# Kernel tuning notes

Hardware: AMD Instinct MI355X
Metric: run time of the kernel (lower is better)

Reference implementation:

```python
import jax, jax.numpy as jnp
import numpy as np

T, B, V, D, H, C = 2048, 32, 50257, 512, 768, 10


def setup_inputs() -> dict:
    key = jax.random.key(0)
    ks = jax.random.split(key, 11)
    s = 0.02
    return {
        "x": jax.random.randint(ks[0], (T, B), 0, V),
        "embed_table": jax.random.normal(ks[1], (V, D), jnp.float32) * s,
        "W_x": jax.random.normal(ks[2], (H, D), jnp.float32) * s,
        "W_f": jax.random.normal(ks[3], (H, D), jnp.float32) * s,
        "b_f": jax.random.normal(ks[4], (H,), jnp.float32) * s,
        "W_r": jax.random.normal(ks[5], (H, D), jnp.float32) * s,
        "b_r": jax.random.normal(ks[6], (H,), jnp.float32) * s,
        "W_cx": jax.random.normal(ks[7], (H, D), jnp.float32) * s,
        "b_cx": jax.random.normal(ks[8], (H,), jnp.float32) * s,
        "W_out": jax.random.normal(ks[9], (C, H), jnp.float32) * s,
        "b_out": jax.random.normal(ks[10], (C,), jnp.float32) * s,
    }


def reference(x, embed_table, W_x, W_f, b_f, W_r, b_r, W_cx, b_cx, W_out, b_out):
    # Embedding lookup: [T, B, D]
    e = embed_table[x]
    # Precompute all gate projections for every timestep (batched GEMMs).
    xp = jnp.einsum("tbd,hd->tbh", e, W_x)                 # x_t projection
    f = jax.nn.sigmoid(jnp.einsum("tbd,hd->tbh", e, W_f) + b_f)   # forget gate
    r = jax.nn.sigmoid(jnp.einsum("tbd,hd->tbh", e, W_r) + b_r)   # reset gate
    cx = jnp.einsum("tbd,hd->tbh", e, W_cx) + b_cx                # highway path

    c0 = jnp.zeros((B, H), e.dtype)  # init_hidden: zeros

    def step(c, inp):
        f_t, xp_t, r_t, cx_t = inp
        c = f_t * c + (1.0 - f_t) * xp_t
        h = r_t * jnp.tanh(c) + (1.0 - r_t) * cx_t
        return c, h

    _, ht = jax.lax.scan(step, c0, (f, xp, r, cx))  # ht: [T, B, H]

    # tanh -> max-pool over time -> tanh -> classifier
    pooled = jnp.max(jnp.tanh(ht), axis=0)          # [B, H]
    pooled = jnp.tanh(pooled)
    logit = pooled @ W_out.T + b_out                # [B, C]
    return logit
```

## Files before the change

kernel.cpp:

```cpp
#include <hip/hip_runtime.h>
#include <hip/hip_bf16.h>
#include <cstdint>
#include <cstddef>

#define T_DIM 2048
#define B_DIM 32
#define D_DIM 512
#define H_DIM 768
#define C_DIM 10
#define K_DIM D_DIM
#define N_DIM (4 * H_DIM)

#define TC 1024
#define NCHUNK (T_DIM / TC)
#define MC (TC * B_DIM)

#define L_SEG 64
#define S_SEG (TC / L_SEG)
#define BH (B_DIM * H_DIM)

typedef __attribute__((ext_vector_type(8))) short short8;
typedef __attribute__((ext_vector_type(4))) float float4v;

__device__ inline unsigned short f2bf(float f) {
  unsigned int u = __builtin_bit_cast(unsigned int, f);
  unsigned int r = (u + 0x7FFFu + ((u >> 16) & 1u)) >> 16;
  return (unsigned short)r;
}
__device__ inline float bf2f(unsigned short s) {
  unsigned int u = ((unsigned int)s) << 16;
  return __builtin_bit_cast(float, u);
}
__device__ inline float fast_rcp(float x) { return __builtin_amdgcn_rcpf(x); }
__device__ inline float fast_exp2(float x) { return __builtin_amdgcn_exp2f(x); }
__device__ inline float sigmoid_f(float x) {
  float e = fast_exp2(-1.4426950408889634f * x);
  return fast_rcp(1.0f + e);
}
__device__ inline float tanh_f(float x) {
  float e = fast_exp2(2.885390081777927f * x);
  return 1.0f - 2.0f * fast_rcp(e + 1.0f);
}
__device__ inline void gld16(const unsigned short* g, unsigned short* l) {
  __builtin_amdgcn_global_load_lds(
      (const __attribute__((address_space(1))) void*)g,
      (__attribute__((address_space(3))) void*)l, 16, 0, 0);
}
__device__ inline unsigned int pack_bf16x2(float lo, float hi) {
  return ((unsigned int)f2bf(hi) << 16) | (unsigned int)f2bf(lo);
}

__global__ __launch_bounds__(256) void gather_embed_kernel(
    const int* __restrict__ x_c, const float* __restrict__ table,
    unsigned short* __restrict__ ebfc) {
  int idx = blockIdx.x * 256 + threadIdx.x;
  int m = idx >> 7;
  int k4 = (idx & 127) << 2;
  int row = x_c[m];
  float4 v = *(const float4*)(table + (size_t)row * D_DIM + k4);
  ushort4 o;
  o.x = f2bf(v.x); o.y = f2bf(v.y); o.z = f2bf(v.z); o.w = f2bf(v.w);
  *(ushort4*)(ebfc + (size_t)m * D_DIM + k4) = o;
}

__global__ __launch_bounds__(256) void convert_w_kernel(
    const float* __restrict__ Wx, const float* __restrict__ Wf,
    const float* __restrict__ Wr, const float* __restrict__ Wcx,
    unsigned short* __restrict__ wcat) {
  int idx = blockIdx.x * 256 + threadIdx.x;
  int n = idx >> 7;
  int k4 = (idx & 127) << 2;
  int mat = n / H_DIM;
  int h = n - mat * H_DIM;
  const float* src = (mat == 0) ? Wx : (mat == 1) ? Wf : (mat == 2) ? Wr : Wcx;
  float4 v = *(const float4*)(src + (size_t)h * D_DIM + k4);
  ushort4 o;
  o.x = f2bf(v.x); o.y = f2bf(v.y); o.z = f2bf(v.z); o.w = f2bf(v.w);
  *(ushort4*)(wcat + (size_t)n * D_DIM + k4) = o;
}

#define BMT 128
#define BNT 256
#define BKT 32
#define NT (K_DIM / BKT)
#define BUF_SH 12288

__device__ __forceinline__ float4v mfma16(short8 a, short8 b, float4v c) {
  return __builtin_amdgcn_mfma_f32_16x16x32_bf16(a, b, c, 0, 0, 0);
}

__device__ __forceinline__ void stgA(const unsigned short* srcA, unsigned short* sm,
                                     int buf, int kt, int tid) {
  const unsigned short* s = srcA + kt * BKT;
  unsigned short* d = sm + buf * BUF_SH + tid * 8;
  gld16(s, d);
  gld16(s + (size_t)128 * K_DIM, d + 4096);
}
__device__ __forceinline__ void stgB(const unsigned short* srcB, unsigned short* sm,
                                     int buf, int kt, int tid) {
  gld16(srcB + kt * BKT, sm + buf * BUF_SH + 8192 + tid * 8);
}

template <int STG, int VMN>
__device__ __forceinline__ void tile_step(
    int u, unsigned short* sm, const unsigned short* srcA,
    const unsigned short* srcB, int tid, int aO, int bO,
    float4v (&acc)[4][4]) {
  unsigned short* c = sm + (u % 3) * BUF_SH;
  const int sbuf = (u + 2) % 3;
  short8 a[4], b[4];
#pragma unroll
  for (int f = 0; f < 4; f++) a[f] = *(const short8*)(c + aO + f * 512);
  b[0] = *(const short8*)(c + bO);
  b[1] = *(const short8*)(c + bO + 512);
  if constexpr (STG) stgA(srcA, sm, sbuf, u + 2, tid);
  __builtin_amdgcn_sched_barrier(0);
  __builtin_amdgcn_s_barrier();
  __builtin_amdgcn_s_setprio(1);
#pragma unroll
  for (int f = 0; f < 4; f++) {
    acc[f][0] = mfma16(a[f], b[0], acc[f][0]);
    acc[f][1] = mfma16(a[f], b[1], acc[f][1]);
  }
  __builtin_amdgcn_s_setprio(0);
  __builtin_amdgcn_sched_barrier(0);
  b[2] = *(const short8*)(c + bO + 1024);
  b[3] = *(const short8*)(c + bO + 1536);
  if constexpr (STG) stgB(srcB, sm, sbuf, u + 2, tid);
  __builtin_amdgcn_sched_barrier(0);
  __builtin_amdgcn_s_setprio(1);
#pragma unroll
  for (int f = 0; f < 4; f++) {
    acc[f][2] = mfma16(a[f], b[2], acc[f][2]);
    acc[f][3] = mfma16(a[f], b[3], acc[f][3]);
  }
  __builtin_amdgcn_s_setprio(0);
  __builtin_amdgcn_sched_barrier(0);
  if constexpr (VMN == 3)
    asm volatile("s_waitcnt vmcnt(3)" ::: "memory");
  else if constexpr (VMN == 0)
    asm volatile("s_waitcnt vmcnt(0)" ::: "memory");
  __builtin_amdgcn_s_barrier();
}

__global__ __launch_bounds__(512, 4) void gemm_kernel(
    const unsigned short* __restrict__ ebfc,
    const unsigned short* __restrict__ wcat,
    const float* __restrict__ b_f, const float* __restrict__ b_r,
    const float* __restrict__ b_cx,
    unsigned short* __restrict__ projc) {
  __shared__ __align__(16) unsigned short smem[36864];

  const int tid = threadIdx.x;
  const int wave = tid >> 6;
  const int lane = tid & 63;
  const int quad = lane >> 4;
  const int l16 = lane & 15;
  const int wn = wave >> 1;
  const int wm = wave & 1;

  const int orig = blockIdx.x;
  const int swz = (orig & 7) * 384 + (orig >> 3);
  const int n_idx = swz % 12;
  const int m_idx = swz / 12;
  const int n0 = n_idx * BNT;
  const int m0 = m_idx * BMT;

  const int arow = tid >> 2;
  const int kchx = (tid & 3) ^ ((arow >> 1) & 3);
  const unsigned short* srcA = wcat + (size_t)(n0 + arow) * K_DIM + kchx * 8;
  const unsigned short* srcB = ebfc + (size_t)(m0 + arow) * K_DIM + kchx * 8;

  const int xr = (quad ^ ((l16 >> 1) & 3)) * 8;
  const int aO = (wn * 64 + l16) * 32 + xr;
  const int bO = 8192 + (wm * 64 + l16) * 32 + xr;

  float4v acc[4][4] = {};

  stgA(srcA, smem, 0, 0, tid);
  stgB(srcB, smem, 0, 0, tid);
  stgA(srcA, smem, 1, 1, tid);
  stgB(srcB, smem, 1, 1, tid);
  asm volatile("s_waitcnt vmcnt(3)" ::: "memory");
  __builtin_amdgcn_s_barrier();

#pragma unroll
  for (int u = 0; u < NT - 2; u++)
    tile_step<1, 3>(u, smem, srcA, srcB, tid, aO, bO, acc);
  tile_step<0, 0>(NT - 2, smem, srcA, srcB, tid, aO, bO, acc);
  tile_step<0, -1>(NT - 1, smem, srcA, srcB, tid, aO, bO, acc);

  __syncthreads();
  int mat = n0 / H_DIM;
  int hb = n0 - mat * H_DIM;
  size_t matBase = (size_t)mat * MC * H_DIM;
  const float* bias = (mat == 1) ? b_f : (mat == 2) ? b_r : b_cx;
#pragma unroll
  for (int f = 0; f < 4; f++) {
    int hl = wn * 64 + f * 16 + quad * 4;
    float4 bv;
    if (mat == 0) { bv.x = bv.y = bv.z = bv.w = 0.0f; }
    else          { bv = *(const float4*)(bias + hb + hl); }
#pragma unroll
    for (int g = 0; g < 4; g++) {
      int ml = wm * 64 + g * 16 + l16;
      float v0 = acc[f][g][0] + bv.x;
      float v1 = acc[f][g][1] + bv.y;
      float v2 = acc[f][g][2] + bv.z;
      float v3 = acc[f][g][3] + bv.w;
      if (mat == 1 || mat == 2) {
        v0 = sigmoid_f(v0); v1 = sigmoid_f(v1);
        v2 = sigmoid_f(v2); v3 = sigmoid_f(v3);
      }
      uint2 pk;
      pk.x = pack_bf16x2(v0, v1);
      pk.y = pack_bf16x2(v2, v3);
      int log8 = hl >> 2;
      int phys8 = log8 ^ ((ml & 7) << 1);
      *(uint2*)(smem + ml * 256 + phys8 * 4) = pk;
    }
  }
  __syncthreads();
#pragma unroll
  for (int it = 0; it < 8; it++) {
    int idx = it * 512 + tid;
    int ml = idx >> 5;
    int c16 = idx & 31;
    int phys16 = c16 ^ (ml & 7);
    short8 v = *(const short8*)(smem + ml * 256 + phys16 * 8);
    *(short8*)(projc + matBase + (size_t)(m0 + ml) * H_DIM + hb + c16 * 8) = v;
  }
}

__global__ __launch_bounds__(128) void scan1_kernel(
    const unsigned short* __restrict__ projc,
    float* __restrict__ Pw, float* __restrict__ Qw) {
  int blk = blockIdx.x;
  int seg = blk / (BH / 512);
  int q   = blk % (BH / 512);
  int e4  = (q * 128 + threadIdx.x) * 4;
  const size_t mstr = (size_t)MC * H_DIM;
  size_t idx0 = (size_t)(seg * L_SEG) * BH + e4;
  float p0 = 1.f, p1 = 1.f, p2 = 1.f, p3 = 1.f;
  float c0 = 0.f, c1 = 0.f, c2 = 0.f, c3 = 0.f;
#pragma unroll 4
  for (int t = 0; t < L_SEG; t++) {
    size_t id = idx0 + (size_t)t * BH;
    ushort4 xp = *(const ushort4*)(projc + id);
    ushort4 ff = *(const ushort4*)(projc + mstr + id);
    float f0 = bf2f(ff.x), f1 = bf2f(ff.y), f2 = bf2f(ff.z), f3 = bf2f(ff.w);
    c0 = fmaf(f0, c0 - bf2f(xp.x), bf2f(xp.x));
    c1 = fmaf(f1, c1 - bf2f(xp.y), bf2f(xp.y));
    c2 = fmaf(f2, c2 - bf2f(xp.z), bf2f(xp.z));
    c3 = fmaf(f3, c3 - bf2f(xp.w), bf2f(xp.w));
    p0 *= f0; p1 *= f1; p2 *= f2; p3 *= f3;
  }
  int o = seg * BH + e4;
  *(float4*)(Pw + o) = make_float4(p0, p1, p2, p3);
  *(float4*)(Qw + o) = make_float4(c0, c1, c2, c3);
}

__global__ __launch_bounds__(256) void prefix_kernel(
    const float* __restrict__ Pw, const float* __restrict__ Qw,
    float* __restrict__ cin, float* __restrict__ c_state,
    const float* __restrict__ segmax, float* __restrict__ hm_state,
    int first, int hm_init) {
  int gid = blockIdx.x * 256 + threadIdx.x;
  float c = first ? 0.f : c_state[gid];
#pragma unroll
  for (int s = 0; s < S_SEG; s++) {
    cin[s * BH + gid] = c;
    c = fmaf(Pw[s * BH + gid], c, Qw[s * BH + gid]);
  }
  c_state[gid] = c;
  if (!first) {
    float m = segmax[gid];
#pragma unroll
    for (int s = 1; s < S_SEG; s++) m = fmaxf(m, segmax[s * BH + gid]);
    hm_state[gid] = hm_init ? m : fmaxf(hm_state[gid], m);
  }
}

__global__ __launch_bounds__(128) void scan2_kernel(
    const unsigned short* __restrict__ projc,
    const float* __restrict__ cin, float* __restrict__ segmax) {
  int blk = blockIdx.x;
  int seg = blk / (BH / 512);
  int q   = blk % (BH / 512);
  int e4  = (q * 128 + threadIdx.x) * 4;
  const size_t mstr = (size_t)MC * H_DIM;
  size_t idx0 = (size_t)(seg * L_SEG) * BH + e4;
  int o = seg * BH + e4;
  float4 cv = *(const float4*)(cin + o);
  float c0 = cv.x, c1 = cv.y, c2 = cv.z, c3 = cv.w;
  float m0 = -1e30f, m1 = -1e30f, m2 = -1e30f, m3 = -1e30f;
#pragma unroll 2
  for (int t = 0; t < L_SEG; t++) {
    size_t id = idx0 + (size_t)t * BH;
    ushort4 xp = *(const ushort4*)(projc + id);
    ushort4 ff = *(const ushort4*)(projc + mstr + id);
    ushort4 rr = *(const ushort4*)(projc + 2 * mstr + id);
    ushort4 cx = *(const ushort4*)(projc + 3 * mstr + id);
    c0 = fmaf(bf2f(ff.x), c0 - bf2f(xp.x), bf2f(xp.x));
    c1 = fmaf(bf2f(ff.y), c1 - bf2f(xp.y), bf2f(xp.y));
    c2 = fmaf(bf2f(ff.z), c2 - bf2f(xp.z), bf2f(xp.z));
    c3 = fmaf(bf2f(ff.w), c3 - bf2f(xp.w), bf2f(xp.w));
    float h0 = fmaf(bf2f(rr.x), tanh_f(c0) - bf2f(cx.x), bf2f(cx.x));
    float h1 = fmaf(bf2f(rr.y), tanh_f(c1) - bf2f(cx.y), bf2f(cx.y));
    float h2 = fmaf(bf2f(rr.z), tanh_f(c2) - bf2f(cx.z), bf2f(cx.z));
    float h3 = fmaf(bf2f(rr.w), tanh_f(c3) - bf2f(cx.w), bf2f(cx.w));
    m0 = fmaxf(m0, h0); m1 = fmaxf(m1, h1);
    m2 = fmaxf(m2, h2); m3 = fmaxf(m3, h3);
  }
  *(float4*)(segmax + o) = make_float4(m0, m1, m2, m3);
}

__global__ __launch_bounds__(256) void pool_final_kernel(
    const float* __restrict__ segmax, const float* __restrict__ hm_state,
    float* __restrict__ pooled) {
  int gid = blockIdx.x * 256 + threadIdx.x;
  float m = hm_state[gid];
#pragma unroll
  for (int s = 0; s < S_SEG; s++) m = fmaxf(m, segmax[s * BH + gid]);
  pooled[gid] = tanh_f(tanh_f(m));
}

__global__ __launch_bounds__(64) void classifier_kernel(
    const float* __restrict__ pooled, const float* __restrict__ W_out,
    const float* __restrict__ b_out, float* __restrict__ out) {
  int b = blockIdx.x / C_DIM;
  int c = blockIdx.x % C_DIM;
  int lane = threadIdx.x;
  float s = 0.0f;
#pragma unroll
  for (int i = 0; i < H_DIM / 64; i++) {
    int h = i * 64 + lane;
    s += pooled[(size_t)b * H_DIM + h] * W_out[(size_t)c * H_DIM + h];
  }
#pragma unroll
  for (int off = 32; off; off >>= 1) s += __shfl_down(s, off, 64);
  if (lane == 0) out[b * C_DIM + c] = s + b_out[c];
}

extern "C" void kernel_launch(void* const* d_in, const int* in_sizes, int n_in,
                              void* d_out, int out_size, void* d_ws, size_t ws_size,
                              hipStream_t stream) {
  const int*   x     = (const int*)d_in[0];
  const float* table = (const float*)d_in[1];
  const float* W_x   = (const float*)d_in[2];
  const float* W_f   = (const float*)d_in[3];
  const float* b_f   = (const float*)d_in[4];
  const float* W_r   = (const float*)d_in[5];
  const float* b_r   = (const float*)d_in[6];
  const float* W_cx  = (const float*)d_in[7];
  const float* b_cx  = (const float*)d_in[8];
  const float* W_out = (const float*)d_in[9];
  const float* b_out = (const float*)d_in[10];

  char* ws = (char*)d_ws;
  size_t off = 0;
  unsigned short* wcat  = (unsigned short*)(ws + off); off += (size_t)N_DIM * K_DIM * 2;
  unsigned short* ebfc  = (unsigned short*)(ws + off); off += (size_t)MC * K_DIM * 2;
  unsigned short* projc = (unsigned short*)(ws + off); off += (size_t)4 * MC * H_DIM * 2;
  float* Pw     = (float*)(ws + off); off += (size_t)S_SEG * BH * 4;
  float* Qw     = (float*)(ws + off); off += (size_t)S_SEG * BH * 4;
  float* cin    = (float*)(ws + off); off += (size_t)S_SEG * BH * 4;
  float* segmax = (float*)(ws + off); off += (size_t)S_SEG * BH * 4;
  float* c_st   = (float*)(ws + off); off += (size_t)BH * 4;
  float* hm_st  = (float*)(ws + off); off += (size_t)BH * 4;
  float* pooled = (float*)(ws + off); off += (size_t)BH * 4;

  convert_w_kernel<<<(N_DIM * K_DIM / 4) / 256, 256, 0, stream>>>(W_x, W_f, W_r, W_cx, wcat);

  for (int ch = 0; ch < NCHUNK; ch++) {
    gather_embed_kernel<<<(MC * K_DIM / 4) / 256, 256, 0, stream>>>(x + (size_t)ch * MC, table, ebfc);
    gemm_kernel<<<(N_DIM / BNT) * (MC / BMT), 512, 0, stream>>>(ebfc, wcat, b_f, b_r, b_cx, projc);
    scan1_kernel<<<S_SEG * (BH / 512), 128, 0, stream>>>(projc, Pw, Qw);
    prefix_kernel<<<BH / 256, 256, 0, stream>>>(Pw, Qw, cin, c_st, segmax, hm_st,
                                                ch == 0, ch == 1);
    scan2_kernel<<<S_SEG * (BH / 512), 128, 0, stream>>>(projc, cin, segmax);
  }
  pool_final_kernel<<<BH / 256, 256, 0, stream>>>(segmax, hm_st, pooled);
  classifier_kernel<<<B_DIM * C_DIM, 64, 0, stream>>>(pooled, W_out, b_out, (float*)d_out);
}
```

Baseline: 522.3 us.

## Reshape GEMM tile to 256x128 with 4 waves each computing 64x128

Changes the projection GEMM block tile from 128(N)x256(M) with 8 waves to 128(N)x256(M)-swapped layout with 4 waves. Each wave now holds a 4x8 accumulator grid, which doubles the MFMA work per LDS A-fragment load. Staging loads, waitcnt counts and the epilogue swizzle are reworked to match. This trades lower wave count and occupancy and higher register pressure for better register-level reuse.

```diff
diff --git a/kernel.cpp b/kernel.cpp
--- a/kernel.cpp
+++ b/kernel.cpp
@@ -79,8 +79,8 @@
   *(ushort4*)(wcat + (size_t)n * D_DIM + k4) = o;
 }
 
-#define BMT 128
-#define BNT 256
+#define BMT 256
+#define BNT 128
 #define BKT 32
 #define NT (K_DIM / BKT)
 #define BUF_SH 12288
@@ -94,56 +94,61 @@
   const unsigned short* s = srcA + kt * BKT;
   unsigned short* d = sm + buf * BUF_SH + tid * 8;
   gld16(s, d);
-  gld16(s + (size_t)128 * K_DIM, d + 4096);
+  gld16(s + (size_t)64 * K_DIM, d + 2048);
 }
 __device__ __forceinline__ void stgB(const unsigned short* srcB, unsigned short* sm,
                                      int buf, int kt, int tid) {
-  gld16(srcB + kt * BKT, sm + buf * BUF_SH + 8192 + tid * 8);
+  const unsigned short* s = srcB + kt * BKT;
+  unsigned short* d = sm + buf * BUF_SH + 4096 + tid * 8;
+  gld16(s, d);
+  gld16(s + (size_t)64 * K_DIM, d + 2048);
+  gld16(s + (size_t)128 * K_DIM, d + 4096);
+  gld16(s + (size_t)192 * K_DIM, d + 6144);
 }
 
 template <int STG, int VMN>
 __device__ __forceinline__ void tile_step(
     int u, unsigned short* sm, const unsigned short* srcA,
     const unsigned short* srcB, int tid, int aO, int bO,
-    float4v (&acc)[4][4]) {
+    float4v (&acc)[4][8]) {
   unsigned short* c = sm + (u % 3) * BUF_SH;
   const int sbuf = (u + 2) % 3;
-  short8 a[4], b[4];
+  short8 a[4], b[8];
 #pragma unroll
   for (int f = 0; f < 4; f++) a[f] = *(const short8*)(c + aO + f * 512);
-  b[0] = *(const short8*)(c + bO);
-  b[1] = *(const short8*)(c + bO + 512);
+#pragma unroll
+  for (int g = 0; g < 4; g++) b[g] = *(const short8*)(c + bO + g * 512);
   if constexpr (STG) stgA(srcA, sm, sbuf, u + 2, tid);
   __builtin_amdgcn_sched_barrier(0);
   __builtin_amdgcn_s_barrier();
   __builtin_amdgcn_s_setprio(1);
 #pragma unroll
-  for (int f = 0; f < 4; f++) {
-    acc[f][0] = mfma16(a[f], b[0], acc[f][0]);
-    acc[f][1] = mfma16(a[f], b[1], acc[f][1]);
-  }
+  for (int f = 0; f < 4; f++)
+#pragma unroll
+    for (int g = 0; g < 4; g++)
+      acc[f][g] = mfma16(a[f], b[g], acc[f][g]);
   __builtin_amdgcn_s_setprio(0);
   __builtin_amdgcn_sched_barrier(0);
-  b[2] = *(const short8*)(c + bO + 1024);
-  b[3] = *(const short8*)(c + bO + 1536);
+#pragma unroll
+  for (int g = 0; g < 4; g++) b[4 + g] = *(const short8*)(c + bO + (4 + g) * 512);
   if constexpr (STG) stgB(srcB, sm, sbuf, u + 2, tid);
   __builtin_amdgcn_sched_barrier(0);
   __builtin_amdgcn_s_setprio(1);
 #pragma unroll
-  for (int f = 0; f < 4; f++) {
-    acc[f][2] = mfma16(a[f], b[2], acc[f][2]);
-    acc[f][3] = mfma16(a[f], b[3], acc[f][3]);
-  }
+  for (int f = 0; f < 4; f++)
+#pragma unroll
+    for (int g = 0; g < 4; g++)
+      acc[f][4 + g] = mfma16(a[f], b[4 + g], acc[f][4 + g]);
   __builtin_amdgcn_s_setprio(0);
   __builtin_amdgcn_sched_barrier(0);
-  if constexpr (VMN == 3)
-    asm volatile("s_waitcnt vmcnt(3)" ::: "memory");
+  if constexpr (VMN == 6)
+    asm volatile("s_waitcnt vmcnt(6)" ::: "memory");
   else if constexpr (VMN == 0)
     asm volatile("s_waitcnt vmcnt(0)" ::: "memory");
   __builtin_amdgcn_s_barrier();
 }
 
-__global__ __launch_bounds__(512, 4) void gemm_kernel(
+__global__ __launch_bounds__(256, 2) void gemm_kernel(
     const unsigned short* __restrict__ ebfc,
     const unsigned short* __restrict__ wcat,
     const float* __restrict__ b_f, const float* __restrict__ b_r,
@@ -156,13 +161,13 @@
   const int lane = tid & 63;
   const int quad = lane >> 4;
   const int l16 = lane & 15;
-  const int wn = wave >> 1;
-  const int wm = wave & 1;
+  const int wn = wave & 1;
+  const int wm = wave >> 1;
 
   const int orig = blockIdx.x;
   const int swz = (orig & 7) * 384 + (orig >> 3);
-  const int n_idx = swz % 12;
-  const int m_idx = swz / 12;
+  const int n_idx = swz % 24;
+  const int m_idx = swz / 24;
   const int n0 = n_idx * BNT;
   const int m0 = m_idx * BMT;
 
@@ -173,20 +178,20 @@
 
   const int xr = (quad ^ ((l16 >> 1) & 3)) * 8;
   const int aO = (wn * 64 + l16) * 32 + xr;
-  const int bO = 8192 + (wm * 64 + l16) * 32 + xr;
-
-  float4v acc[4][4] = {};
+  const int bO = 4096 + (wm * 128 + l16) * 32 + xr;
+
+  float4v acc[4][8] = {};
 
   stgA(srcA, smem, 0, 0, tid);
   stgB(srcB, smem, 0, 0, tid);
   stgA(srcA, smem, 1, 1, tid);
   stgB(srcB, smem, 1, 1, tid);
-  asm volatile("s_waitcnt vmcnt(3)" ::: "memory");
+  asm volatile("s_waitcnt vmcnt(6)" ::: "memory");
   __builtin_amdgcn_s_barrier();
 
 #pragma unroll
   for (int u = 0; u < NT - 2; u++)
-    tile_step<1, 3>(u, smem, srcA, srcB, tid, aO, bO, acc);
+    tile_step<1, 6>(u, smem, srcA, srcB, tid, aO, bO, acc);
   tile_step<0, 0>(NT - 2, smem, srcA, srcB, tid, aO, bO, acc);
   tile_step<0, -1>(NT - 1, smem, srcA, srcB, tid, aO, bO, acc);
 
@@ -202,8 +207,8 @@
     if (mat == 0) { bv.x = bv.y = bv.z = bv.w = 0.0f; }
     else          { bv = *(const float4*)(bias + hb + hl); }
 #pragma unroll
-    for (int g = 0; g < 4; g++) {
-      int ml = wm * 64 + g * 16 + l16;
+    for (int g = 0; g < 8; g++) {
+      int ml = wm * 128 + g * 16 + l16;
       float v0 = acc[f][g][0] + bv.x;
       float v1 = acc[f][g][1] + bv.y;
       float v2 = acc[f][g][2] + bv.z;
@@ -215,19 +220,18 @@
       uint2 pk;
       pk.x = pack_bf16x2(v0, v1);
       pk.y = pack_bf16x2(v2, v3);
-      int log8 = hl >> 2;
-      int phys8 = log8 ^ ((ml & 7) << 1);
-      *(uint2*)(smem + ml * 256 + phys8 * 4) = pk;
+      int chunk = (hl >> 3) ^ (ml & 7);
+      *(uint2*)(smem + ml * 128 + chunk * 8 + (hl & 7)) = pk;
     }
   }
   __syncthreads();
 #pragma unroll
-  for (int it = 0; it < 8; it++) {
-    int idx = it * 512 + tid;
-    int ml = idx >> 5;
-    int c16 = idx & 31;
-    int phys16 = c16 ^ (ml & 7);
-    short8 v = *(const short8*)(smem + ml * 256 + phys16 * 8);
+  for (int it = 0; it < 16; it++) {
+    int idx = it * 256 + tid;
+    int ml = idx >> 4;
+    int c16 = idx & 15;
+    int phys = c16 ^ (ml & 7);
+    short8 v = *(const short8*)(smem + ml * 128 + phys * 8);
     *(short8*)(projc + matBase + (size_t)(m0 + ml) * H_DIM + hb + c16 * 8) = v;
   }
 }
@@ -374,7 +378,7 @@
 
   for (int ch = 0; ch < NCHUNK; ch++) {
     gather_embed_kernel<<<(MC * K_DIM / 4) / 256, 256, 0, stream>>>(x + (size_t)ch * MC, table, ebfc);
-    gemm_kernel<<<(N_DIM / BNT) * (MC / BMT), 512, 0, stream>>>(ebfc, wcat, b_f, b_r, b_cx, projc);
+    gemm_kernel<<<(N_DIM / BNT) * (MC / BMT), 256, 0, stream>>>(ebfc, wcat, b_f, b_r, b_cx, projc);
     scan1_kernel<<<S_SEG * (BH / 512), 128, 0, stream>>>(projc, Pw, Qw);
     prefix_kernel<<<BH / 256, 256, 0, stream>>>(Pw, Qw, cin, c_st, segmax, hm_st,
                                                 ch == 0, ch == 1);
```

Result: no change. 525.8 us (+0.7%).

## Load GEMM A operand directly from global into registers, keep only B in LDS

Applied to the files above, without the earlier changes.

The weight (A) tiles are now loaded straight from global memory into per-wave registers with a one-step register double buffer, instead of being staged through LDS. Only the embedding (B) tiles stay in a triple-buffered LDS ring, which shrinks shared memory, removes a barrier per k-step and merges the two MFMA halves into one 16-MFMA burst. In exchange each wave issues its own uncoalesced global reads for A, register pressure rises, and launch bounds drop from 4 to 3 blocks per CU.

```diff
diff --git a/kernel.cpp b/kernel.cpp
--- a/kernel.cpp
+++ b/kernel.cpp
@@ -83,73 +83,58 @@
 #define BNT 256
 #define BKT 32
 #define NT (K_DIM / BKT)
-#define BUF_SH 12288
+#define BBUF 4096
 
 __device__ __forceinline__ float4v mfma16(short8 a, short8 b, float4v c) {
   return __builtin_amdgcn_mfma_f32_16x16x32_bf16(a, b, c, 0, 0, 0);
 }
 
-__device__ __forceinline__ void stgA(const unsigned short* srcA, unsigned short* sm,
-                                     int buf, int kt, int tid) {
-  const unsigned short* s = srcA + kt * BKT;
-  unsigned short* d = sm + buf * BUF_SH + tid * 8;
-  gld16(s, d);
-  gld16(s + (size_t)128 * K_DIM, d + 4096);
-}
 __device__ __forceinline__ void stgB(const unsigned short* srcB, unsigned short* sm,
                                      int buf, int kt, int tid) {
-  gld16(srcB + kt * BKT, sm + buf * BUF_SH + 8192 + tid * 8);
-}
-
-template <int STG, int VMN>
+  gld16(srcB + kt * BKT, sm + buf * BBUF + tid * 8);
+}
+
+__device__ __forceinline__ void loadA(const unsigned short* aG, int kt,
+                                      short8 (&a)[4]) {
+#pragma unroll
+  for (int f = 0; f < 4; f++)
+    a[f] = *(const short8*)(aG + (size_t)f * 16 * K_DIM + kt * BKT);
+}
+
+template <int LDA, int STG, int VMN>
 __device__ __forceinline__ void tile_step(
-    int u, unsigned short* sm, const unsigned short* srcA,
-    const unsigned short* srcB, int tid, int aO, int bO,
-    float4v (&acc)[4][4]) {
-  unsigned short* c = sm + (u % 3) * BUF_SH;
-  const int sbuf = (u + 2) % 3;
-  short8 a[4], b[4];
-#pragma unroll
-  for (int f = 0; f < 4; f++) a[f] = *(const short8*)(c + aO + f * 512);
-  b[0] = *(const short8*)(c + bO);
-  b[1] = *(const short8*)(c + bO + 512);
-  if constexpr (STG) stgA(srcA, sm, sbuf, u + 2, tid);
+    int u, unsigned short* sm, const unsigned short* aG,
+    const unsigned short* srcB, int tid, int bO,
+    short8 (&acur)[4], short8 (&anxt)[4], float4v (&acc)[4][4]) {
+  const unsigned short* c = sm + (u % 3) * BBUF;
+  short8 b[4];
+#pragma unroll
+  for (int g = 0; g < 4; g++) b[g] = *(const short8*)(c + bO + g * 512);
+  if constexpr (LDA) loadA(aG, u + 1, anxt);
+  if constexpr (STG) stgB(srcB, sm, (u + 2) % 3, u + 2, tid);
   __builtin_amdgcn_sched_barrier(0);
-  __builtin_amdgcn_s_barrier();
   __builtin_amdgcn_s_setprio(1);
 #pragma unroll
-  for (int f = 0; f < 4; f++) {
-    acc[f][0] = mfma16(a[f], b[0], acc[f][0]);
-    acc[f][1] = mfma16(a[f], b[1], acc[f][1]);
-  }
+  for (int f = 0; f < 4; f++)
+#pragma unroll
+    for (int g = 0; g < 4; g++)
+      acc[f][g] = mfma16(acur[f], b[g], acc[f][g]);
   __builtin_amdgcn_s_setprio(0);
   __builtin_amdgcn_sched_barrier(0);
-  b[2] = *(const short8*)(c + bO + 1024);
-  b[3] = *(const short8*)(c + bO + 1536);
-  if constexpr (STG) stgB(srcB, sm, sbuf, u + 2, tid);
-  __builtin_amdgcn_sched_barrier(0);
-  __builtin_amdgcn_s_setprio(1);
-#pragma unroll
-  for (int f = 0; f < 4; f++) {
-    acc[f][2] = mfma16(a[f], b[2], acc[f][2]);
-    acc[f][3] = mfma16(a[f], b[3], acc[f][3]);
-  }
-  __builtin_amdgcn_s_setprio(0);
-  __builtin_amdgcn_sched_barrier(0);
-  if constexpr (VMN == 3)
-    asm volatile("s_waitcnt vmcnt(3)" ::: "memory");
+  if constexpr (VMN == 1)
+    asm volatile("s_waitcnt vmcnt(1)" ::: "memory");
   else if constexpr (VMN == 0)
     asm volatile("s_waitcnt vmcnt(0)" ::: "memory");
-  __builtin_amdgcn_s_barrier();
-}
-
-__global__ __launch_bounds__(512, 4) void gemm_kernel(
+  if constexpr (VMN >= 0) __builtin_amdgcn_s_barrier();
+}
+
+__global__ __launch_bounds__(512, 3) void gemm_kernel(
     const unsigned short* __restrict__ ebfc,
     const unsigned short* __restrict__ wcat,
     const float* __restrict__ b_f, const float* __restrict__ b_r,
     const float* __restrict__ b_cx,
     unsigned short* __restrict__ projc) {
-  __shared__ __align__(16) unsigned short smem[36864];
+  __shared__ __align__(16) unsigned short smem[32768];
 
   const int tid = threadIdx.x;
   const int wave = tid >> 6;
@@ -168,27 +153,31 @@
 
   const int arow = tid >> 2;
   const int kchx = (tid & 3) ^ ((arow >> 1) & 3);
-  const unsigned short* srcA = wcat + (size_t)(n0 + arow) * K_DIM + kchx * 8;
   const unsigned short* srcB = ebfc + (size_t)(m0 + arow) * K_DIM + kchx * 8;
 
+  const unsigned short* aG = wcat + (size_t)(n0 + wn * 64 + l16) * K_DIM + quad * 8;
+
   const int xr = (quad ^ ((l16 >> 1) & 3)) * 8;
-  const int aO = (wn * 64 + l16) * 32 + xr;
-  const int bO = 8192 + (wm * 64 + l16) * 32 + xr;
+  const int bO = (wm * 64 + l16) * 32 + xr;
 
   float4v acc[4][4] = {};
-
-  stgA(srcA, smem, 0, 0, tid);
+  short8 a0[4], a1[4];
+
   stgB(srcB, smem, 0, 0, tid);
-  stgA(srcA, smem, 1, 1, tid);
+  loadA(aG, 0, a0);
   stgB(srcB, smem, 1, 1, tid);
-  asm volatile("s_waitcnt vmcnt(3)" ::: "memory");
+  __builtin_amdgcn_sched_barrier(0);
+  asm volatile("s_waitcnt vmcnt(1)" ::: "memory");
   __builtin_amdgcn_s_barrier();
 
 #pragma unroll
-  for (int u = 0; u < NT - 2; u++)
-    tile_step<1, 3>(u, smem, srcA, srcB, tid, aO, bO, acc);
-  tile_step<0, 0>(NT - 2, smem, srcA, srcB, tid, aO, bO, acc);
-  tile_step<0, -1>(NT - 1, smem, srcA, srcB, tid, aO, bO, acc);
+  for (int u = 0; u < NT - 2; u += 2) {
+    tile_step<1, 1, 1>(u, smem, aG, srcB, tid, bO, a0, a1, acc);
+    if (u + 1 < NT - 2)
+      tile_step<1, 1, 1>(u + 1, smem, aG, srcB, tid, bO, a1, a0, acc);
+  }
+  tile_step<1, 0, 0>(NT - 2, smem, aG, srcB, tid, bO, a0, a1, acc);
+  tile_step<0, 0, -1>(NT - 1, smem, aG, srcB, tid, bO, a1, a0, acc);
 
   __syncthreads();
   int mat = n0 / H_DIM;
```

After: 834.9 us. 59.8% more time.
